# Kernel tuning notes

Measured on AMD Instinct MI355X. Metric: run time of the kernel, lower is better.

The kernel has to match this reference:

```python
import jax, jax.numpy as jnp
import numpy as np

B, LX, LY, D = 8, 128, 512, 256


def setup_inputs() -> dict:
    key = jax.random.key(0)
    k = jax.random.split(key, 7)
    s1 = 1.0 / np.sqrt(2 * D)
    s2 = 1.0 / np.sqrt(D)
    return {
        "x": jax.random.normal(k[0], (B, LX, D), dtype=jnp.float32),
        "y": jax.random.normal(k[1], (B, LY, D), dtype=jnp.float32),
        "y_mask": jax.random.randint(k[2], (B, LY), 0, 2).astype(bool),
        "W1": jax.random.uniform(k[3], (2 * D, D), jnp.float32, -s1, s1),
        "b1": jax.random.uniform(k[4], (D,), jnp.float32, -s1, s1),
        "W2": jax.random.uniform(k[5], (D, 1), jnp.float32, -s2, s2),
        "b2": jax.random.uniform(k[6], (1,), jnp.float32, -s2, s2),
    }


def reference(x, y, y_mask, W1, b1, W2, b2):
    # Algebraically split the first linear on the concat [x; y]:
    # cat([x,y]) @ W1 == x @ W1[:D] + y @ W1[D:]
    d = x.shape[-1]
    hx = jnp.einsum('bxd,de->bxe', x, W1[:d])            # (B, LX, D)
    hy = jnp.einsum('byd,de->bye', y, W1[d:])            # (B, LY, D)
    h = jax.nn.relu(hx[:, :, None, :] + hy[:, None, :, :] + b1)  # (B, LX, LY, D)
    scores = jnp.einsum('bxyd,d->bxy', h, W2[:, 0]) + b2[0]      # (B, LX, LY)
    scores = jnp.where(y_mask[:, None, :], -jnp.inf, scores)
    weights = jax.nn.softmax(scores, axis=2)
    contexts = jnp.einsum('bxy,byd->bxd', weights, y)    # (B, LX, D)
    return contexts
```

## Files before the change

kernel.cpp:

```cpp
#include <hip/hip_runtime.h>
#include <math.h>

#define BB 8
#define LX 128
#define LY 512
#define DD 256

typedef _Float16 h2t __attribute__((ext_vector_type(2)));

static __device__ __forceinline__ h2t u2h(unsigned int u) {
    h2t r; __builtin_memcpy(&r, &u, 4); return r;
}
static __device__ __forceinline__ unsigned int pk16(float a, float b) {
    h2t h; h.x = (_Float16)a; h.y = (_Float16)b;
    unsigned int u; __builtin_memcpy(&u, &h, 4); return u;
}
static __device__ __forceinline__ h2t rlh(unsigned int v, int l) {
    return u2h((unsigned int)__builtin_amdgcn_readlane((int)v, l));
}

#if defined(__has_builtin) && __has_builtin(__builtin_amdgcn_fdot2)
#define DOT2(a, b, c) __builtin_amdgcn_fdot2((a), (b), (c), false)
#else
#define DOT2(a, b, c) fmaf((float)(a).x, (float)(b).x, fmaf((float)(a).y, (float)(b).y, (c)))
#endif

#define A16_OFF  0
#define CT16_OFF 131072
#define W16_OFF  655360

__global__ __launch_bounds__(256) void gemm_kernel(
    const float* __restrict__ x, const float* __restrict__ y,
    const float* __restrict__ W1, const float* __restrict__ b1,
    const float* __restrict__ W2, float* __restrict__ ws)
{
    __shared__ float sA[32][20];
    __shared__ float sW[32][128];

    const int g  = blockIdx.x;
    const int t  = threadIdx.x;
    const int tc = t & 31;
    const int tr = t >> 5;

    const bool isA = (g < 128);
    const float* inp;
    const float* wbase;
    int row0, col0;
    if (isA) { col0 = (g & 1) * 128;  row0 = (g >> 1) * 16;  inp = x; wbase = W1; }
    else     { int h = g - 128; col0 = (h & 1) * 128; row0 = (h >> 1) * 16; inp = y; wbase = W1 + DD * DD; }

    float acc[2][4];
    #pragma unroll
    for (int i = 0; i < 2; ++i)
        #pragma unroll
        for (int j = 0; j < 4; ++j) acc[i][j] = 0.f;

    for (int k0 = 0; k0 < DD; k0 += 32) {
        __syncthreads();
        if (t < 128) {
            int row = t >> 3, kq = t & 7;
            const float4 v = *(const float4*)(inp + (size_t)(row0 + row) * DD + k0 + 4 * kq);
            sA[4*kq + 0][row] = v.x;
            sA[4*kq + 1][row] = v.y;
            sA[4*kq + 2][row] = v.z;
            sA[4*kq + 3][row] = v.w;
        }
        #pragma unroll
        for (int i = 0; i < 4; ++i) {
            int flat = t + i * 256;
            int kk = flat >> 5, c4 = flat & 31;
            *(float4*)&sW[kk][4*c4] = *(const float4*)(wbase + (size_t)(k0 + kk) * DD + col0 + 4 * c4);
        }
        __syncthreads();
        #pragma unroll
        for (int k = 0; k < 32; ++k) {
            const float a0 = sA[k][2*tr], a1 = sA[k][2*tr + 1];
            const float4 w4 = *(const float4*)&sW[k][4*tc];
            acc[0][0] = fmaf(a0, w4.x, acc[0][0]);
            acc[0][1] = fmaf(a0, w4.y, acc[0][1]);
            acc[0][2] = fmaf(a0, w4.z, acc[0][2]);
            acc[0][3] = fmaf(a0, w4.w, acc[0][3]);
            acc[1][0] = fmaf(a1, w4.x, acc[1][0]);
            acc[1][1] = fmaf(a1, w4.y, acc[1][1]);
            acc[1][2] = fmaf(a1, w4.z, acc[1][2]);
            acc[1][3] = fmaf(a1, w4.w, acc[1][3]);
        }
    }

    const int dq = (col0 >> 2) + tc;
    if (isA) {
        uint2* A16u2 = (uint2*)(ws + A16_OFF);
        const float4 bv = *(const float4*)(b1 + col0 + 4 * tc);
        #pragma unroll
        for (int i = 0; i < 2; ++i) {
            const int r = row0 + 2 * tr + i;
            uint2 st;
            st.x = pk16(acc[i][0] + bv.x, acc[i][1] + bv.y);
            st.y = pk16(acc[i][2] + bv.z, acc[i][3] + bv.w);
            A16u2[(size_t)r * 64 + dq] = st;
        }
        if (g == 0 && t < 64) {
            uint2* W16u2 = (uint2*)(ws + W16_OFF);
            const float4 wv = *(const float4*)(W2 + 4 * t);
            uint2 st;
            st.x = pk16(wv.x, wv.y);
            st.y = pk16(wv.z, wv.w);
            W16u2[t] = st;
        }
    } else {
        uint2* Ct16u2 = (uint2*)(ws + CT16_OFF);
        #pragma unroll
        for (int i = 0; i < 2; ++i) {
            const int ry = row0 + 2 * tr + i;
            const int bb = ry >> 9, yy = ry & 511;
            uint2 st;
            st.x = pk16(acc[i][0], acc[i][1]);
            st.y = pk16(acc[i][2], acc[i][3]);
            Ct16u2[((size_t)(bb * 64 + dq)) * 512 + yy] = st;
        }
    }
}

__global__ __launch_bounds__(512) void fused_kernel(
    const float* __restrict__ yin, const int* __restrict__ ymask,
    const float* __restrict__ b2,
    const uint2* __restrict__ A16, const uint2* __restrict__ Ct,
    const uint2* __restrict__ W16,
    float* __restrict__ out)
{
    __shared__ __align__(16) float pl[LY][4];
    __shared__ __align__(16) float4 Lp[8];

    const int t    = threadIdx.x;
    const int lane = t & 63;
    const int w    = __builtin_amdgcn_readfirstlane(t >> 6);
    const int b    = blockIdx.x & 7;
    const int xg   = blockIdx.x >> 3;
    const int y    = w * 64 + lane;

    const uint2* Ab = A16 + ((size_t)(b * LX + xg * 4)) * 64;
    uint2 av0 = Ab[lane];
    uint2 av1 = Ab[64 + lane];
    uint2 av2 = Ab[128 + lane];
    uint2 av3 = Ab[192 + lane];
    const uint2 wv = W16[lane];

    const uint2* ctb = Ct + ((size_t)b * 64) * 512 + y;
    const float  b2v = b2[0];
    const bool   msk = ymask[(size_t)b * LY + y] != 0;

    float s0 = 0.f, s1 = 0.f, s2 = 0.f, s3 = 0.f;

    #pragma unroll 4
    for (int dq = 0; dq < 64; ++dq) {
        const uint2 cu = ctb[(size_t)dq * 512];
        const h2t c0 = u2h(cu.x), c1 = u2h(cu.y);
        const h2t w0 = rlh(wv.x, dq), w1 = rlh(wv.y, dq);
        h2t zz; zz.x = (_Float16)0.f; zz.y = (_Float16)0.f;
        {
            const h2t a0 = rlh(av0.x, dq), a1 = rlh(av0.y, dq);
            const h2t h0 = __builtin_elementwise_max(a0 + c0, zz);
            const h2t h1 = __builtin_elementwise_max(a1 + c1, zz);
            s0 = DOT2(h0, w0, s0); s0 = DOT2(h1, w1, s0);
        }
        {
            const h2t a0 = rlh(av1.x, dq), a1 = rlh(av1.y, dq);
            const h2t h0 = __builtin_elementwise_max(a0 + c0, zz);
            const h2t h1 = __builtin_elementwise_max(a1 + c1, zz);
            s1 = DOT2(h0, w0, s1); s1 = DOT2(h1, w1, s1);
        }
        {
            const h2t a0 = rlh(av2.x, dq), a1 = rlh(av2.y, dq);
            const h2t h0 = __builtin_elementwise_max(a0 + c0, zz);
            const h2t h1 = __builtin_elementwise_max(a1 + c1, zz);
            s2 = DOT2(h0, w0, s2); s2 = DOT2(h1, w1, s2);
        }
        {
            const h2t a0 = rlh(av3.x, dq), a1 = rlh(av3.y, dq);
            const h2t h0 = __builtin_elementwise_max(a0 + c0, zz);
            const h2t h1 = __builtin_elementwise_max(a1 + c1, zz);
            s3 = DOT2(h0, w0, s3); s3 = DOT2(h1, w1, s3);
        }
    }

    const float p0 = msk ? 0.f : __expf(s0 + b2v);
    const float p1 = msk ? 0.f : __expf(s1 + b2v);
    const float p2 = msk ? 0.f : __expf(s2 + b2v);
    const float p3 = msk ? 0.f : __expf(s3 + b2v);

    float l0 = p0, l1 = p1, l2 = p2, l3 = p3;
    #pragma unroll
    for (int off = 32; off; off >>= 1) {
        l0 += __shfl_xor(l0, off);
        l1 += __shfl_xor(l1, off);
        l2 += __shfl_xor(l2, off);
        l3 += __shfl_xor(l3, off);
    }

    *(float4*)&pl[y][0] = make_float4(p0, p1, p2, p3);
    if (lane == 0) Lp[w] = make_float4(l0, l1, l2, l3);
    __syncthreads();

    const int d  = t & 255;
    const int xh = t >> 8;
    float L0 = 0.f, L1 = 0.f;
    #pragma unroll
    for (int ww = 0; ww < 8; ++ww) {
        const float4 lv = Lp[ww];
        L0 += xh ? lv.z : lv.x;
        L1 += xh ? lv.w : lv.y;
    }

    float a0 = 0.f, a1 = 0.f;
    const float* Yb = yin + (size_t)b * LY * DD + d;
    #pragma unroll 8
    for (int yy = 0; yy < LY; ++yy) {
        const float v = Yb[(size_t)yy * DD];
        const float2 pp = *(const float2*)&pl[yy][2 * xh];
        a0 = fmaf(pp.x, v, a0);
        a1 = fmaf(pp.y, v, a1);
    }

    const size_t row = (size_t)(b * LX + xg * 4 + 2 * xh);
    out[row * DD + d]       = a0 / L0;
    out[(row + 1) * DD + d] = a1 / L1;
}

extern "C" void kernel_launch(void* const* d_in, const int* in_sizes, int n_in,
                              void* d_out, int out_size, void* d_ws, size_t ws_size,
                              hipStream_t stream) {
    const float* x     = (const float*)d_in[0];
    const float* y     = (const float*)d_in[1];
    const int*   ymask = (const int*)  d_in[2];
    const float* W1    = (const float*)d_in[3];
    const float* b1    = (const float*)d_in[4];
    const float* W2    = (const float*)d_in[5];
    const float* b2    = (const float*)d_in[6];
    float* ws  = (float*)d_ws;
    float* out = (float*)d_out;

    hipLaunchKernelGGL(gemm_kernel, dim3(640), dim3(256), 0, stream, x, y, W1, b1, W2, ws);
    hipLaunchKernelGGL(fused_kernel, dim3(256), dim3(512), 0, stream,
                       y, ymask, b2,
                       (const uint2*)(ws + A16_OFF), (const uint2*)(ws + CT16_OFF),
                       (const uint2*)(ws + W16_OFF), out);
}
```

Before: 46.08 us.

## Convert y to packed fp16 pairs and use fdot2 for context accumulation

```diff
diff --git a/kernel.cpp b/kernel.cpp
--- a/kernel.cpp
+++ b/kernel.cpp
@@ -28,17 +28,35 @@
 #define A16_OFF  0
 #define CT16_OFF 131072
 #define W16_OFF  655360
+#define Y16_OFF  655488
 
 __global__ __launch_bounds__(256) void gemm_kernel(
     const float* __restrict__ x, const float* __restrict__ y,
     const float* __restrict__ W1, const float* __restrict__ b1,
     const float* __restrict__ W2, float* __restrict__ ws)
 {
+    const int g = blockIdx.x;
+    const int t = threadIdx.x;
+
+    if (g >= 640) {
+        const int g2 = g - 640;
+        const int bb = g2 >> 3;
+        const int yy0 = (g2 & 7) * 32;
+        unsigned int* Yp = (unsigned int*)(ws + Y16_OFF);
+        const float* yb = y + (size_t)bb * LY * DD;
+        #pragma unroll 4
+        for (int i = 0; i < 32; ++i) {
+            const int yy = yy0 + i;
+            const float v0 = yb[(size_t)(2 * yy) * DD + t];
+            const float v1 = yb[(size_t)(2 * yy + 1) * DD + t];
+            Yp[((size_t)(bb * 256) + yy) * 256 + t] = pk16(v0, v1);
+        }
+        return;
+    }
+
     __shared__ float sA[32][20];
     __shared__ float sW[32][128];
 
-    const int g  = blockIdx.x;
-    const int t  = threadIdx.x;
     const int tc = t & 31;
     const int tr = t >> 5;
 
@@ -122,13 +140,12 @@
 }
 
 __global__ __launch_bounds__(512) void fused_kernel(
-    const float* __restrict__ yin, const int* __restrict__ ymask,
-    const float* __restrict__ b2,
+    const int* __restrict__ ymask, const float* __restrict__ b2,
     const uint2* __restrict__ A16, const uint2* __restrict__ Ct,
-    const uint2* __restrict__ W16,
+    const uint2* __restrict__ W16, const unsigned int* __restrict__ Y16p,
     float* __restrict__ out)
 {
-    __shared__ __align__(16) float pl[LY][4];
+    __shared__ __align__(16) unsigned int pp[256][4];
     __shared__ __align__(16) float4 Lp[8];
 
     const int t    = threadIdx.x;
@@ -150,13 +167,13 @@
     const bool   msk = ymask[(size_t)b * LY + y] != 0;
 
     float s0 = 0.f, s1 = 0.f, s2 = 0.f, s3 = 0.f;
+    h2t zz; zz.x = (_Float16)0.f; zz.y = (_Float16)0.f;
 
     #pragma unroll 4
     for (int dq = 0; dq < 64; ++dq) {
         const uint2 cu = ctb[(size_t)dq * 512];
         const h2t c0 = u2h(cu.x), c1 = u2h(cu.y);
         const h2t w0 = rlh(wv.x, dq), w1 = rlh(wv.y, dq);
-        h2t zz; zz.x = (_Float16)0.f; zz.y = (_Float16)0.f;
         {
             const h2t a0 = rlh(av0.x, dq), a1 = rlh(av0.y, dq);
             const h2t h0 = __builtin_elementwise_max(a0 + c0, zz);
@@ -197,7 +214,18 @@
         l3 += __shfl_xor(l3, off);
     }
 
-    *(float4*)&pl[y][0] = make_float4(p0, p1, p2, p3);
+    const float q0 = __shfl_xor(p0, 1);
+    const float q1 = __shfl_xor(p1, 1);
+    const float q2 = __shfl_xor(p2, 1);
+    const float q3 = __shfl_xor(p3, 1);
+    if (!(lane & 1)) {
+        uint4 st;
+        st.x = pk16(p0, q0);
+        st.y = pk16(p1, q1);
+        st.z = pk16(p2, q2);
+        st.w = pk16(p3, q3);
+        *(uint4*)&pp[y >> 1][0] = st;
+    }
     if (lane == 0) Lp[w] = make_float4(l0, l1, l2, l3);
     __syncthreads();
 
@@ -212,13 +240,13 @@
     }
 
     float a0 = 0.f, a1 = 0.f;
-    const float* Yb = yin + (size_t)b * LY * DD + d;
+    const unsigned int* Yb = Y16p + ((size_t)b * 256) * 256 + d;
     #pragma unroll 8
-    for (int yy = 0; yy < LY; ++yy) {
-        const float v = Yb[(size_t)yy * DD];
-        const float2 pp = *(const float2*)&pl[yy][2 * xh];
-        a0 = fmaf(pp.x, v, a0);
-        a1 = fmaf(pp.y, v, a1);
+    for (int yy = 0; yy < 256; ++yy) {
+        const h2t v = u2h(Yb[(size_t)yy * 256]);
+        const uint2 pv = *(const uint2*)&pp[yy][2 * xh];
+        a0 = DOT2(u2h(pv.x), v, a0);
+        a1 = DOT2(u2h(pv.y), v, a1);
     }
 
     const size_t row = (size_t)(b * LX + xg * 4 + 2 * xh);
@@ -239,9 +267,10 @@
     float* ws  = (float*)d_ws;
     float* out = (float*)d_out;
 
-    hipLaunchKernelGGL(gemm_kernel, dim3(640), dim3(256), 0, stream, x, y, W1, b1, W2, ws);
+    hipLaunchKernelGGL(gemm_kernel, dim3(704), dim3(256), 0, stream, x, y, W1, b1, W2, ws);
     hipLaunchKernelGGL(fused_kernel, dim3(256), dim3(512), 0, stream,
-                       y, ymask, b2,
+                       ymask, b2,
                        (const uint2*)(ws + A16_OFF), (const uint2*)(ws + CT16_OFF),
-                       (const uint2*)(ws + W16_OFF), out);
-}
+                       (const uint2*)(ws + W16_OFF), (const unsigned int*)(ws + Y16_OFF),
+                       out);
+}
```

New measurement: 47.27 us. 2.6% more time.
